# Kernel tuning notes

Hardware: AMD Instinct MI355X
Metric: run time of the kernel (lower is better)

## Reference

```python
import jax, jax.numpy as jnp
import numpy as np

D_MODEL = 768
NUM_HEADS = 12
D_K = D_MODEL // NUM_HEADS
D_FF = 2048
LN_EPS = 1e-3  # Keras LayerNormalization default
B, S = 4, 2048


def layer_norm(x, gamma, beta):
    mu = jnp.mean(x, axis=-1, keepdims=True)
    var = jnp.var(x, axis=-1, keepdims=True)
    return (x - mu) * jax.lax.rsqrt(var + LN_EPS) * gamma + beta


def setup_inputs() -> dict:
    key = jax.random.key(0)
    ks = jax.random.split(key, 16)
    sd = 0.02
    inp = {
        "x": jax.random.normal(ks[0], (B, S, D_MODEL), dtype=jnp.float32),
        "src_mask": jnp.zeros((B, 1, 1, S), dtype=jnp.float32),
        "Wq": jax.random.normal(ks[1], (D_MODEL, D_MODEL), jnp.float32) * sd,
        "bq": jnp.zeros((D_MODEL,), jnp.float32),
        "Wk": jax.random.normal(ks[2], (D_MODEL, D_MODEL), jnp.float32) * sd,
        "bk": jnp.zeros((D_MODEL,), jnp.float32),
        "Wv": jax.random.normal(ks[3], (D_MODEL, D_MODEL), jnp.float32) * sd,
        "bv": jnp.zeros((D_MODEL,), jnp.float32),
        "Wo": jax.random.normal(ks[4], (D_MODEL, D_MODEL), jnp.float32) * sd,
        "bo": jnp.zeros((D_MODEL,), jnp.float32),
        "W1": jax.random.normal(ks[5], (D_MODEL, D_FF), jnp.float32) * sd,
        "b1": jnp.zeros((D_FF,), jnp.float32),
        "W2": jax.random.normal(ks[6], (D_FF, D_MODEL), jnp.float32) * sd,
        "b2": jnp.zeros((D_MODEL,), jnp.float32),
        "gamma1": jnp.ones((D_MODEL,), jnp.float32),
        "beta1": jnp.zeros((D_MODEL,), jnp.float32),
        "gamma2": jnp.ones((D_MODEL,), jnp.float32),
        "beta2": jnp.zeros((D_MODEL,), jnp.float32),
    }
    return inp


def encoder_layer(x, src_mask, Wq, bq, Wk, bk, Wv, bv, Wo, bo, W1, b1, W2, b2,
                  gamma1, beta1, gamma2, beta2):
    b, s, _ = x.shape
    def heads(t):  # [B,S,D] -> [B,H,S,Dk]
        return t.reshape(b, s, NUM_HEADS, D_K).transpose(0, 2, 1, 3)
    Q = heads(x @ Wq + bq)
    K = heads(x @ Wk + bk)
    V = heads(x @ Wv + bv)
    scores = jnp.einsum("bhqd,bhkd->bhqk", Q, K) / jnp.sqrt(jnp.float32(D_K))
    scores = scores + src_mask * (-1e9)
    probs = jax.nn.softmax(scores, axis=-1)
    attn = jnp.einsum("bhqk,bhkd->bhqd", probs, V)
    attn = attn.transpose(0, 2, 1, 3).reshape(b, s, D_MODEL)
    attn_out = attn @ Wo + bo
    # dropout is identity at inference
    x1 = layer_norm(x + attn_out, gamma1, beta1)
    ff = jax.nn.relu(x1 @ W1 + b1) @ W2 + b2
    return layer_norm(x1 + ff, gamma2, beta2)


def reference(x, src_mask, Wq, bq, Wk, bk, Wv, bv, Wo, bo, W1, b1, W2, b2,
              gamma1, beta1, gamma2, beta2):
    return encoder_layer(x, src_mask, Wq, bq, Wk, bk, Wv, bv, Wo, bo,
                         W1, b1, W2, b2, gamma1, beta1, gamma2, beta2)
```

## Files before the change

### kernel.cpp

```cpp
#include <hip/hip_runtime.h>


typedef unsigned short u16;
typedef __bf16 bf16x8 __attribute__((ext_vector_type(8)));
typedef __bf16 bf16x4 __attribute__((ext_vector_type(4)));
typedef unsigned short u16x8 __attribute__((ext_vector_type(8)));
typedef float f32x4 __attribute__((ext_vector_type(4)));

#define D_MODEL 768
#define D_FF    2048
#define NH      12
#define DK      64
#define S_LEN   2048
#define M_TOK   8192

#define QSCALE   0.18033688011112042f
#define MSCALE  -1.4426950408889634e9f

__device__ __forceinline__ float bf2f(u16 v) {
    union { unsigned u; float f; } c; c.u = ((unsigned)v) << 16; return c.f;
}
__device__ __forceinline__ void st_bf(u16* p, float v) { *(__bf16*)p = (__bf16)v; }

__device__ __forceinline__ void gload_lds16(const void* g, void* l) {
    __builtin_amdgcn_global_load_lds(
        (const __attribute__((address_space(1))) void*)g,
        (__attribute__((address_space(3))) void*)l, 16, 0, 0);
}

__global__ __launch_bounds__(256)
void prep_k(const float* __restrict__ x, const float* __restrict__ Wq,
            const float* __restrict__ Wk, const float* __restrict__ Wv,
            const float* __restrict__ Wo, const float* __restrict__ W1,
            const float* __restrict__ W2, u16* __restrict__ xb,
            u16* __restrict__ WqkvT, u16* __restrict__ WoT,
            u16* __restrict__ W1T, u16* __restrict__ W2T) {
    __shared__ float t[32][33];
    const int id = blockIdx.x, tid = threadIdx.x;
    if (id >= 5376) {
        const int i = ((id - 5376) * 256 + tid) * 4;
        const float4 v = *(const float4*)(x + i);
        __bf16 o[4] = {(__bf16)v.x, (__bf16)v.y, (__bf16)v.z, (__bf16)v.w};
        *(bf16x4*)(xb + i) = *(bf16x4*)o;
        return;
    }
    const float* in; u16* out; int R, C, bx, by;
    if (id < 2304) {
        const int z = id / 576, r = id % 576;
        in = z == 0 ? Wq : (z == 1 ? Wk : (z == 2 ? Wv : Wo));
        out = z == 3 ? WoT : WqkvT + z * 768 * 768;
        R = 768; C = 768; bx = (r % 24) * 32; by = (r / 24) * 32;
    } else if (id < 3840) {
        const int r = id - 2304;
        in = W1; out = W1T; R = 768; C = 2048;
        bx = (r % 64) * 32; by = (r / 64) * 32;
    } else {
        const int r = id - 3840;
        in = W2; out = W2T; R = 2048; C = 768;
        bx = (r % 24) * 32; by = (r / 24) * 32;
    }
    const int tx = tid & 31, ty = tid >> 5;
#pragma unroll
    for (int i = 0; i < 32; i += 8)
        t[ty + i][tx] = in[(size_t)(by + ty + i) * C + bx + tx];
    __syncthreads();
#pragma unroll
    for (int i = 0; i < 32; i += 8)
        st_bf(&out[(size_t)(bx + ty + i) * R + by + tx], t[tx][ty + i]);
}

__global__ __launch_bounds__(256, 3)
void qkv_gemm_k(const u16* __restrict__ A, const u16* __restrict__ Bt,
                const float* __restrict__ bq, const float* __restrict__ bk,
                const float* __restrict__ bv, u16* __restrict__ Qb,
                u16* __restrict__ Kb, u16* __restrict__ Vt) {
    __shared__ __align__(16) u16 As[2][128 * 32];
    __shared__ __align__(16) u16 Bs[2][128 * 32];
    const int tid = threadIdx.x;
    const int lane = tid & 63, w = tid >> 6;
    const int r16 = lane & 15, qd = lane >> 4;
    const int qdx = (qd ^ ((r16 >> 1) & 3)) << 3;
    const int m0 = blockIdx.x * 128, n0 = blockIdx.y * 128;
    const int wm = (w & 1) << 6, wn = (w >> 1) << 6;
    const int K = D_MODEL;

    f32x4 acc[4][4] = {};

    const u16* aP[2]; const u16* bP[2]; int f8[2];
#pragma unroll
    for (int it = 0; it < 2; ++it) {
        const int f = it * 256 + tid;
        const int row = f >> 2;
        const int kc = ((f & 3) ^ ((f >> 3) & 3)) << 3;
        aP[it] = A  + (size_t)(m0 + row) * K + kc;
        bP[it] = Bt + (size_t)(n0 + row) * K + kc;
        f8[it] = f * 8;
    }

    for (int k0 = 0; k0 < K; k0 += 64) {
#pragma unroll
        for (int p = 0; p < 2; ++p)
#pragma unroll
            for (int it = 0; it < 2; ++it) {
                gload_lds16(aP[it] + k0 + p * 32, &As[p][f8[it]]);
                gload_lds16(bP[it] + k0 + p * 32, &Bs[p][f8[it]]);
            }
        __syncthreads();
#pragma unroll
        for (int p = 0; p < 2; ++p) {
            bf16x8 af[4], bfr[4];
#pragma unroll
            for (int i = 0; i < 4; ++i) {
                af[i]  = *(const bf16x8*)&As[p][(wm + i * 16 + r16) * 32 + qdx];
                bfr[i] = *(const bf16x8*)&Bs[p][(wn + i * 16 + r16) * 32 + qdx];
            }
#pragma unroll
            for (int i = 0; i < 4; ++i)
#pragma unroll
                for (int j = 0; j < 4; ++j)
                    acc[i][j] = __builtin_amdgcn_mfma_f32_16x16x32_bf16(af[i], bfr[j], acc[i][j], 0, 0, 0);
        }
        __syncthreads();
    }

    const int sel = n0 < 768 ? 0 : (n0 < 1536 ? 1 : 2);
    const float* bias = sel == 0 ? bq : (sel == 1 ? bk : bv);
    const float scale = sel == 0 ? QSCALE : 1.0f;
    const int nbase = n0 - sel * 768;

#pragma unroll
    for (int j = 0; j < 4; ++j) {
        const int ncol = nbase + wn + j * 16 + r16;
        const float bvv = bias[ncol];
#pragma unroll
        for (int i = 0; i < 4; ++i) {
            if (sel == 2) {
                const int h = ncol >> 6, d = ncol & 63;
                const int mb = m0 + wm + i * 16 + qd * 4;
                const int bb = mb >> 11, npb = mb & 2047;
                __bf16 pk[4];
#pragma unroll
                for (int rr = 0; rr < 4; ++rr) pk[rr] = (__bf16)(acc[i][j][rr] + bvv);
                *(bf16x4*)&Vt[(((size_t)(bb * NH + h)) * DK + d) * S_LEN + npb] = *(bf16x4*)pk;
            } else {
#pragma unroll
                for (int rr = 0; rr < 4; ++rr) {
                    const int m = m0 + wm + i * 16 + qd * 4 + rr;
                    const float v = (acc[i][j][rr] + bvv) * scale;
                    if (sel == 0) st_bf(&Qb[(size_t)m * D_MODEL + ncol], v);
                    else          st_bf(&Kb[(size_t)m * D_MODEL + ncol], v);
                }
            }
        }
    }
}

__global__ __launch_bounds__(256, 2)
void g4p_k(const u16* __restrict__ A, const u16* __restrict__ Bt,
           const float* __restrict__ bias, u16* __restrict__ Cout,
           int N, int K) {
    __shared__ __align__(16) u16 AB[2][16384];
    const int tid = threadIdx.x, lane = tid & 63;
    const int w = tid >> 6;
    const int wm2 = w >> 1, wn2 = w & 1;
    const int r16 = lane & 15, qd = lane >> 4;
    const int qdx = (qd ^ ((r16 >> 1) & 3)) << 3;
    const int m0 = blockIdx.x * 128, n0 = blockIdx.y * 128;
    const int NT = K >> 6;

    const u16* aS[4]; const u16* bS[4];
#pragma unroll
    for (int l = 0; l < 4; ++l) {
        const int f = l * 256 + tid;
        const int row = (f >> 2) & 127, ks = f >> 9;
        const int e = (((f & 3) ^ ((f >> 3) & 3)) << 3);
        aS[l] = A  + (size_t)(m0 + row) * K + ks * 32 + e;
        bS[l] = Bt + (size_t)(n0 + row) * K + ks * 32 + e;
    }

#pragma unroll
    for (int l = 0; l < 4; ++l) {
        gload_lds16(aS[l], &AB[0][(l * 256 + tid) * 8]);
        gload_lds16(bS[l], &AB[0][8192 + (l * 256 + tid) * 8]);
    }
    asm volatile("s_waitcnt vmcnt(0)" ::: "memory");
    __builtin_amdgcn_s_barrier();

    f32x4 acc[4][4] = {};
    bf16x8 af[4][2], bfr[4][2];
    const int arow0 = wm2 * 64 + r16;
    const int brow0 = wn2 * 64 + r16;

    for (int t = 0; t < NT; ++t) {
        const int cur = t & 1, nxt = cur ^ 1;
        const u16* ab = AB[cur];
        const int ka = (t + 1) * 64;
        const bool more = (t + 1) < NT;

#pragma unroll
        for (int mt = 0; mt < 4; ++mt)
#pragma unroll
            for (int ks = 0; ks < 2; ++ks)
                af[mt][ks] = *(const bf16x8*)&ab[ks * 4096 + (arow0 + mt * 16) * 32 + qdx];
#pragma unroll
        for (int nt = 0; nt < 2; ++nt)
#pragma unroll
            for (int ks = 0; ks < 2; ++ks)
                bfr[nt][ks] = *(const bf16x8*)&ab[8192 + ks * 4096 + (brow0 + nt * 16) * 32 + qdx];
        if (more) {
#pragma unroll
            for (int l = 0; l < 4; ++l)
                gload_lds16(aS[l] + ka, &AB[nxt][(l * 256 + tid) * 8]);
        }
        __builtin_amdgcn_s_setprio(1);
#pragma unroll
        for (int mt = 0; mt < 4; ++mt)
#pragma unroll
            for (int nt = 0; nt < 2; ++nt)
#pragma unroll
                for (int ks = 0; ks < 2; ++ks)
                    acc[mt][nt] = __builtin_amdgcn_mfma_f32_16x16x32_bf16(bfr[nt][ks], af[mt][ks], acc[mt][nt], 0, 0, 0);
        __builtin_amdgcn_s_setprio(0);
        __builtin_amdgcn_s_barrier();

#pragma unroll
        for (int nt = 2; nt < 4; ++nt)
#pragma unroll
            for (int ks = 0; ks < 2; ++ks)
                bfr[nt][ks] = *(const bf16x8*)&ab[8192 + ks * 4096 + (brow0 + nt * 16) * 32 + qdx];
        if (more) {
#pragma unroll
            for (int l = 0; l < 4; ++l)
                gload_lds16(bS[l] + ka, &AB[nxt][8192 + (l * 256 + tid) * 8]);
        }
        __builtin_amdgcn_s_setprio(1);
#pragma unroll
        for (int mt = 0; mt < 4; ++mt)
#pragma unroll
            for (int nt = 2; nt < 4; ++nt)
#pragma unroll
                for (int ks = 0; ks < 2; ++ks)
                    acc[mt][nt] = __builtin_amdgcn_mfma_f32_16x16x32_bf16(bfr[nt][ks], af[mt][ks], acc[mt][nt], 0, 0, 0);
        __builtin_amdgcn_s_setprio(0);

        if (more) {
            asm volatile("s_waitcnt vmcnt(0)" ::: "memory");
            __builtin_amdgcn_s_barrier();
        }
    }

#pragma unroll
    for (int nt = 0; nt < 4; ++nt) {
        const int nb = n0 + wn2 * 64 + nt * 16 + qd * 4;
        const float4 bv = *(const float4*)&bias[nb];
        const float b4[4] = {bv.x, bv.y, bv.z, bv.w};
#pragma unroll
        for (int mi = 0; mi < 4; ++mi) {
            const int m = m0 + wm2 * 64 + mi * 16 + r16;
            __bf16 pk[4];
#pragma unroll
            for (int rr = 0; rr < 4; ++rr)
                pk[rr] = (__bf16)(acc[mi][nt][rr] + b4[rr]);
            *(bf16x4*)&Cout[(size_t)m * N + nb] = *(bf16x4*)pk;
        }
    }
}

__global__ __launch_bounds__(512, 2)
void ff1_k(const u16* __restrict__ A, const u16* __restrict__ Bt,
           const float* __restrict__ bias, u16* __restrict__ C) {
    __shared__ __align__(16) u16 AB[2][32768];
    const int tid = threadIdx.x, lane = tid & 63;
    const int w = tid >> 6;
    const int wm2 = w >> 2, wn4 = w & 3;
    const int r16 = lane & 15, qd = lane >> 4;
    const int qdx = (qd ^ ((r16 >> 1) & 3)) << 3;
    const int m0 = blockIdx.x * 256, n0 = blockIdx.y * 256;
    const int K = D_MODEL, NT = 12;

    const u16* aS[4]; const u16* bS[4];
#pragma unroll
    for (int l = 0; l < 4; ++l) {
        const int f = l * 512 + tid;
        const int row = (f >> 2) & 255, ks = f >> 10;
        const int e = (((f & 3) ^ ((f >> 3) & 3)) << 3);
        aS[l] = A  + (size_t)(m0 + row) * K + ks * 32 + e;
        bS[l] = Bt + (size_t)(n0 + row) * K + ks * 32 + e;
    }

#pragma unroll
    for (int l = 0; l < 4; ++l) {
        gload_lds16(aS[l], &AB[0][(l * 512 + tid) * 8]);
        gload_lds16(bS[l], &AB[0][16384 + (l * 512 + tid) * 8]);
    }
    asm volatile("s_waitcnt vmcnt(0)" ::: "memory");
    __builtin_amdgcn_s_barrier();

    f32x4 acc[8][4] = {};
    bf16x8 af[4][2], bfr[4][2];
    const int arow0 = wm2 * 128 + r16;
    const int brow0 = wn4 * 64 + r16;

    for (int t = 0; t < NT; ++t) {
        const int cur = t & 1, nxt = cur ^ 1;
        const u16* ab = AB[cur];
        const int ka = (t + 1) * 64;
        const bool more = (t + 1) < NT;

#pragma unroll
        for (int mt = 0; mt < 4; ++mt)
#pragma unroll
            for (int ks = 0; ks < 2; ++ks)
                af[mt][ks] = *(const bf16x8*)&ab[ks * 8192 + (arow0 + mt * 16) * 32 + qdx];
#pragma unroll
        for (int nt = 0; nt < 2; ++nt)
#pragma unroll
            for (int ks = 0; ks < 2; ++ks)
                bfr[nt][ks] = *(const bf16x8*)&ab[16384 + ks * 8192 + (brow0 + nt * 16) * 32 + qdx];
        if (more) {
#pragma unroll
            for (int l = 0; l < 4; ++l)
                gload_lds16(aS[l] + ka, &AB[nxt][(l * 512 + tid) * 8]);
        }
        __builtin_amdgcn_s_setprio(1);
#pragma unroll
        for (int mt = 0; mt < 4; ++mt)
#pragma unroll
            for (int nt = 0; nt < 2; ++nt)
#pragma unroll
                for (int ks = 0; ks < 2; ++ks)
                    acc[mt][nt] = __builtin_amdgcn_mfma_f32_16x16x32_bf16(bfr[nt][ks], af[mt][ks], acc[mt][nt], 0, 0, 0);
        __builtin_amdgcn_s_setprio(0);
        __builtin_amdgcn_s_barrier();

#pragma unroll
        for (int nt = 2; nt < 4; ++nt)
#pragma unroll
            for (int ks = 0; ks < 2; ++ks)
                bfr[nt][ks] = *(const bf16x8*)&ab[16384 + ks * 8192 + (brow0 + nt * 16) * 32 + qdx];
        if (more) {
#pragma unroll
            for (int l = 0; l < 4; ++l)
                gload_lds16(bS[l] + ka, &AB[nxt][16384 + (l * 512 + tid) * 8]);
        }
        __builtin_amdgcn_s_setprio(1);
#pragma unroll
        for (int mt = 0; mt < 4; ++mt)
#pragma unroll
            for (int nt = 2; nt < 4; ++nt)
#pragma unroll
                for (int ks = 0; ks < 2; ++ks)
                    acc[mt][nt] = __builtin_amdgcn_mfma_f32_16x16x32_bf16(bfr[nt][ks], af[mt][ks], acc[mt][nt], 0, 0, 0);
        __builtin_amdgcn_s_setprio(0);
        __builtin_amdgcn_s_barrier();

#pragma unroll
        for (int mt = 0; mt < 4; ++mt)
#pragma unroll
            for (int ks = 0; ks < 2; ++ks)
                af[mt][ks] = *(const bf16x8*)&ab[ks * 8192 + (arow0 + 64 + mt * 16) * 32 + qdx];
        __builtin_amdgcn_s_setprio(1);
#pragma unroll
        for (int mt = 0; mt < 4; ++mt)
#pragma unroll
            for (int nt = 0; nt < 2; ++nt)
#pragma unroll
                for (int ks = 0; ks < 2; ++ks)
                    acc[4 + mt][nt] = __builtin_amdgcn_mfma_f32_16x16x32_bf16(bfr[nt][ks], af[mt][ks], acc[4 + mt][nt], 0, 0, 0);
        __builtin_amdgcn_s_setprio(0);
        __builtin_amdgcn_s_barrier();

        __builtin_amdgcn_s_setprio(1);
#pragma unroll
        for (int mt = 0; mt < 4; ++mt)
#pragma unroll
            for (int nt = 2; nt < 4; ++nt)
#pragma unroll
                for (int ks = 0; ks < 2; ++ks)
                    acc[4 + mt][nt] = __builtin_amdgcn_mfma_f32_16x16x32_bf16(bfr[nt][ks], af[mt][ks], acc[4 + mt][nt], 0, 0, 0);
        __builtin_amdgcn_s_setprio(0);

        if (more) {
            asm volatile("s_waitcnt vmcnt(0)" ::: "memory");
            __builtin_amdgcn_s_barrier();
        }
    }

#pragma unroll
    for (int nt = 0; nt < 4; ++nt) {
        const int nb = n0 + wn4 * 64 + nt * 16 + qd * 4;
        const float4 bv = *(const float4*)&bias[nb];
        const float b4[4] = {bv.x, bv.y, bv.z, bv.w};
#pragma unroll
        for (int mi = 0; mi < 8; ++mi) {
            const int m = m0 + wm2 * 128 + (mi >> 2) * 64 + (mi & 3) * 16 + r16;
            __bf16 pk[4];
#pragma unroll
            for (int rr = 0; rr < 4; ++rr)
                pk[rr] = (__bf16)fmaxf(acc[mi][nt][rr] + b4[rr], 0.0f);
            *(bf16x4*)&C[(size_t)m * D_FF + nb] = *(bf16x4*)pk;
        }
    }
}

#define TS 72

__global__ __launch_bounds__(256, 3)
void attn_k(const u16* __restrict__ Qg, const u16* __restrict__ Kg,
            const u16* __restrict__ Vtg, const float* __restrict__ maskg,
            u16* __restrict__ Og) {
    const int tid = threadIdx.x, lane = tid & 63, w = tid >> 6;
    const int qh = w & 1, kh = w >> 1;
    const int r16 = lane & 15, qd = lane >> 4;
    const int q0 = blockIdx.x * 128;
    const int h = blockIdx.y, b = blockIdx.z;

    __shared__ __align__(16) u16 sm[(64 + 64 + 128) * TS];
    u16* Ks  = sm;
    u16* Vts = sm + 64 * TS;
    u16* Ps  = sm + 128 * TS;

    bf16x8 qa[4][2];
#pragma unroll
    for (int mt = 0; mt < 4; ++mt)
#pragma unroll
        for (int ks = 0; ks < 2; ++ks)
            qa[mt][ks] = *(const bf16x8*)(Qg +
                ((size_t)((b * S_LEN + q0 + qh * 64 + mt * 16 + r16) * NH + h)) * DK +
                ks * 32 + qd * 8);

    const int srow = tid >> 3, sc = (tid & 7) << 3;
    const u16* vsrc = Vtg + (((size_t)(b * NH + h)) * DK) * S_LEN;
    u16x8 kreg[2], vreg[2];
#pragma unroll
    for (int it = 0; it < 2; ++it) {
        const int row = srow + it * 32;
        kreg[it] = *(const u16x8*)(Kg + ((size_t)((b * S_LEN + row) * NH + h)) * DK + sc);
        vreg[it] = *(const u16x8*)(vsrc + (size_t)row * S_LEN + sc);
    }

    float l_i[4] = {0.0f, 0.0f, 0.0f, 0.0f};
    f32x4 Oacc[4][4] = {};

    for (int kt = 0; kt < S_LEN / 64; ++kt) {
        const int ks0 = kt * 64;

#pragma unroll
        for (int it = 0; it < 2; ++it) {
            const int row = srow + it * 32;
            *(u16x8*)&Ks[row * TS + sc]  = kreg[it];
            *(u16x8*)&Vts[row * TS + sc] = vreg[it];
        }

        float4 mrow[2];
#pragma unroll
        for (int nt = 0; nt < 2; ++nt) {
            const float4 mm = ((const float4*)(maskg + (size_t)b * S_LEN + ks0))[kh * 8 + nt * 4 + qd];
            mrow[nt].x = mm.x * MSCALE; mrow[nt].y = mm.y * MSCALE;
            mrow[nt].z = mm.z * MSCALE; mrow[nt].w = mm.w * MSCALE;
        }
        __syncthreads();

        f32x4 sa[4][2];
#pragma unroll
        for (int mt = 0; mt < 4; ++mt)
#pragma unroll
            for (int nt = 0; nt < 2; ++nt) {
                sa[mt][nt][0] = mrow[nt].x; sa[mt][nt][1] = mrow[nt].y;
                sa[mt][nt][2] = mrow[nt].z; sa[mt][nt][3] = mrow[nt].w;
            }
#pragma unroll
        for (int ks = 0; ks < 2; ++ks) {
            bf16x8 kb[2];
#pragma unroll
            for (int nt = 0; nt < 2; ++nt)
                kb[nt] = *(const bf16x8*)&Ks[(kh * 32 + nt * 16 + r16) * TS + ks * 32 + qd * 8];
            __builtin_amdgcn_s_setprio(1);
#pragma unroll
            for (int mt = 0; mt < 4; ++mt)
#pragma unroll
                for (int nt = 0; nt < 2; ++nt)
                    sa[mt][nt] = __builtin_amdgcn_mfma_f32_16x16x32_bf16(kb[nt], qa[mt][ks], sa[mt][nt], 0, 0, 0);
            __builtin_amdgcn_s_setprio(0);
        }

#pragma unroll
        for (int mt = 0; mt < 4; ++mt) {
            float rsum = 0.0f;
#pragma unroll
            for (int nt = 0; nt < 2; ++nt) {
                sa[mt][nt][0] = __builtin_amdgcn_exp2f(sa[mt][nt][0]);
                sa[mt][nt][1] = __builtin_amdgcn_exp2f(sa[mt][nt][1]);
                sa[mt][nt][2] = __builtin_amdgcn_exp2f(sa[mt][nt][2]);
                sa[mt][nt][3] = __builtin_amdgcn_exp2f(sa[mt][nt][3]);
                rsum += sa[mt][nt][0] + sa[mt][nt][1] + sa[mt][nt][2] + sa[mt][nt][3];
            }
            rsum += __shfl_xor(rsum, 16);
            rsum += __shfl_xor(rsum, 32);
            l_i[mt] += rsum;
        }

#pragma unroll
        for (int mt = 0; mt < 4; ++mt)
#pragma unroll
            for (int nt = 0; nt < 2; ++nt) {
                __bf16 pk[4];
#pragma unroll
                for (int rr = 0; rr < 4; ++rr) pk[rr] = (__bf16)sa[mt][nt][rr];
                *(bf16x4*)&Ps[(qh * 64 + mt * 16 + r16) * TS + kh * 32 + nt * 16 + qd * 4] = *(bf16x4*)pk;
            }

        if (kt + 1 < S_LEN / 64) {
            const int ns0 = ks0 + 64;
#pragma unroll
            for (int it = 0; it < 2; ++it) {
                const int row = srow + it * 32;
                kreg[it] = *(const u16x8*)(Kg + ((size_t)((b * S_LEN + ns0 + row) * NH + h)) * DK + sc);
                vreg[it] = *(const u16x8*)(vsrc + (size_t)row * S_LEN + ns0 + sc);
            }
        }

        {
            bf16x8 pa[4], vb[4];
#pragma unroll
            for (int mt = 0; mt < 4; ++mt)
                pa[mt] = *(const bf16x8*)&Ps[(qh * 64 + mt * 16 + r16) * TS + kh * 32 + qd * 8];
#pragma unroll
            for (int vt = 0; vt < 4; ++vt)
                vb[vt] = *(const bf16x8*)&Vts[(vt * 16 + r16) * TS + kh * 32 + qd * 8];
            __builtin_amdgcn_s_setprio(1);
#pragma unroll
            for (int mt = 0; mt < 4; ++mt)
#pragma unroll
                for (int vt = 0; vt < 4; ++vt)
                    Oacc[mt][vt] = __builtin_amdgcn_mfma_f32_16x16x32_bf16(pa[mt], vb[vt], Oacc[mt][vt], 0, 0, 0);
            __builtin_amdgcn_s_setprio(0);
        }
        __syncthreads();
    }

    __syncthreads();
    float* mb  = (float*)sm;
    float* lsm = mb + 128 * 64;
    if (kh == 0) {
#pragma unroll
        for (int mt = 0; mt < 4; ++mt) {
            if (qd == 0) lsm[(qh * 4 + mt) * 16 + r16] = l_i[mt];
#pragma unroll
            for (int vt = 0; vt < 4; ++vt)
#pragma unroll
                for (int rr = 0; rr < 4; ++rr)
                    mb[(qh * 64 + mt * 16 + qd * 4 + rr) * 64 + vt * 16 + r16] = Oacc[mt][vt][rr];
        }
    }
    __syncthreads();
    if (kh == 1) {
#pragma unroll
        for (int mt = 0; mt < 4; ++mt) {
            const float linv = 1.0f / (l_i[mt] + lsm[(qh * 4 + mt) * 16 + r16]);
#pragma unroll
            for (int rr = 0; rr < 4; ++rr) {
                const float lr = __shfl(linv, qd * 4 + rr);
                const int qrow = q0 + qh * 64 + mt * 16 + qd * 4 + rr;
#pragma unroll
                for (int vt = 0; vt < 4; ++vt) {
                    const float o = Oacc[mt][vt][rr] +
                        mb[(qh * 64 + mt * 16 + qd * 4 + rr) * 64 + vt * 16 + r16];
                    st_bf(&Og[((size_t)((b * S_LEN + qrow) * NH + h)) * DK + vt * 16 + r16],
                          o * lr);
                }
            }
        }
    }
}

__global__ __launch_bounds__(256, 4)
void resln_k(const u16* __restrict__ xb, const u16* __restrict__ yb,
             const float* __restrict__ gamma, const float* __restrict__ beta,
             u16* __restrict__ outb, float* __restrict__ outf) {
    const int row = blockIdx.x, tid = threadIdx.x;
    const int lane = tid & 63, w = tid >> 6;
    __shared__ float redS[4], redS2[4];
    const size_t base = (size_t)row * D_MODEL;
    float h[3], s = 0.0f, s2 = 0.0f;
#pragma unroll
    for (int i = 0; i < 3; ++i) {
        const int c = i * 256 + tid;
        const float v = bf2f(xb[base + c]) + bf2f(yb[base + c]);
        h[i] = v; s += v; s2 += v * v;
    }
#pragma unroll
    for (int off = 32; off >= 1; off >>= 1) { s += __shfl_xor(s, off); s2 += __shfl_xor(s2, off); }
    if (lane == 0) { redS[w] = s; redS2[w] = s2; }
    __syncthreads();
    s  = redS[0] + redS[1] + redS[2] + redS[3];
    s2 = redS2[0] + redS2[1] + redS2[2] + redS2[3];
    const float mu  = s * (1.0f / D_MODEL);
    const float var = s2 * (1.0f / D_MODEL) - mu * mu;
    const float rstd = rsqrtf(var + 1e-3f);
#pragma unroll
    for (int i = 0; i < 3; ++i) {
        const int c = i * 256 + tid;
        const float o = (h[i] - mu) * rstd * gamma[c] + beta[c];
        if (outb) st_bf(&outb[base + c], o);
        if (outf) outf[base + c] = o;
    }
}

extern "C" void kernel_launch(void* const* d_in, const int* in_sizes, int n_in,
                              void* d_out, int out_size, void* d_ws, size_t ws_size,
                              hipStream_t stream) {
    (void)in_sizes; (void)n_in; (void)out_size; (void)ws_size;
    const float* x    = (const float*)d_in[0];
    const float* mask = (const float*)d_in[1];
    const float* Wq = (const float*)d_in[2];  const float* bq  = (const float*)d_in[3];
    const float* Wk = (const float*)d_in[4];  const float* bk  = (const float*)d_in[5];
    const float* Wv = (const float*)d_in[6];  const float* bv  = (const float*)d_in[7];
    const float* Wo = (const float*)d_in[8];  const float* bo  = (const float*)d_in[9];
    const float* W1 = (const float*)d_in[10]; const float* b1  = (const float*)d_in[11];
    const float* W2 = (const float*)d_in[12]; const float* b2  = (const float*)d_in[13];
    const float* g1 = (const float*)d_in[14]; const float* be1 = (const float*)d_in[15];
    const float* g2 = (const float*)d_in[16]; const float* be2 = (const float*)d_in[17];

    char* ws = (char*)d_ws;
    u16* xb     = (u16*)(ws + 0);
    u16* WqkvT  = (u16*)(ws + 12582912);
    u16* WoT    = (u16*)(ws + 16121856);
    u16* W1T    = (u16*)(ws + 17301504);
    u16* W2T    = (u16*)(ws + 20447232);
    u16* Qb     = (u16*)(ws + 23592960);
    u16* Kb     = (u16*)(ws + 36175872);
    u16* Vtg    = (u16*)(ws + 48758784);
    u16* Ab     = (u16*)(ws + 61341696);
    u16* Yb     = (u16*)(ws + 73924608);
    u16* X1b    = (u16*)(ws + 86507520);
    u16* H1b    = (u16*)(ws + 23592960);
    u16* Y2b    = (u16*)(ws + 73924608);

    const dim3 blk(256);

    prep_k<<<dim3(11520), blk, 0, stream>>>(x, Wq, Wk, Wv, Wo, W1, W2,
                                            xb, WqkvT, WoT, W1T, W2T);

    qkv_gemm_k<<<dim3(64, 18), blk, 0, stream>>>(xb, WqkvT, bq, bk, bv, Qb, Kb, Vtg);

    attn_k<<<dim3(16, NH, 4), blk, 0, stream>>>(Qb, Kb, Vtg, mask, Ab);

    g4p_k<<<dim3(64, 6), blk, 0, stream>>>(Ab, WoT, bo, Yb, D_MODEL, D_MODEL);

    resln_k<<<dim3(M_TOK), blk, 0, stream>>>(xb, Yb, g1, be1, X1b, nullptr);

    ff1_k<<<dim3(32, 8), dim3(512), 0, stream>>>(X1b, W1T, b1, H1b);

    g4p_k<<<dim3(64, 6), blk, 0, stream>>>(H1b, W2T, b2, Y2b, D_MODEL, D_FF);

    resln_k<<<dim3(M_TOK), blk, 0, stream>>>(X1b, Y2b, g2, be2, nullptr, (float*)d_out);
}
```

Before: 330.5 us.

## Double-buffer QKV GEMM with split-phase prefetch and swapped MFMA operands

Replaces the QKV projection GEMM with a double-buffered, two-phase pipelined version modeled on the existing g4p_k. It prefetches the next K-tile into the alternate LDS buffer while MFMAs run on the current one, and uses s_setprio around the MFMA blocks. MFMA operands are swapped so each lane holds four consecutive output columns, which allows vectorized bias loads and bf16x4 stores for Q and K. The cost is that V transposed stores become scalar, and occupancy drops from 3 to 2 blocks per CU because of the larger LDS buffer.

```diff
diff --git a/kernel.cpp b/kernel.cpp
--- a/kernel.cpp
+++ b/kernel.cpp
@@ -69,58 +69,99 @@
         st_bf(&out[(size_t)(bx + ty + i) * R + by + tx], t[tx][ty + i]);
 }
 
-__global__ __launch_bounds__(256, 3)
-void qkv_gemm_k(const u16* __restrict__ A, const u16* __restrict__ Bt,
-                const float* __restrict__ bq, const float* __restrict__ bk,
-                const float* __restrict__ bv, u16* __restrict__ Qb,
-                u16* __restrict__ Kb, u16* __restrict__ Vt) {
-    __shared__ __align__(16) u16 As[2][128 * 32];
-    __shared__ __align__(16) u16 Bs[2][128 * 32];
-    const int tid = threadIdx.x;
-    const int lane = tid & 63, w = tid >> 6;
+__global__ __launch_bounds__(256, 2)
+void qkv4p_k(const u16* __restrict__ A, const u16* __restrict__ Bt,
+             const float* __restrict__ bq, const float* __restrict__ bk,
+             const float* __restrict__ bv, u16* __restrict__ Qb,
+             u16* __restrict__ Kb, u16* __restrict__ Vt) {
+    __shared__ __align__(16) u16 AB[2][16384];
+    const int tid = threadIdx.x, lane = tid & 63;
+    const int w = tid >> 6;
+    const int wm2 = w >> 1, wn2 = w & 1;
     const int r16 = lane & 15, qd = lane >> 4;
     const int qdx = (qd ^ ((r16 >> 1) & 3)) << 3;
     const int m0 = blockIdx.x * 128, n0 = blockIdx.y * 128;
-    const int wm = (w & 1) << 6, wn = (w >> 1) << 6;
-    const int K = D_MODEL;
+    const int K = D_MODEL, NT = 12;
+
+    const u16* aS[4]; const u16* bS[4];
+#pragma unroll
+    for (int l = 0; l < 4; ++l) {
+        const int f = l * 256 + tid;
+        const int row = (f >> 2) & 127, ks = f >> 9;
+        const int e = (((f & 3) ^ ((f >> 3) & 3)) << 3);
+        aS[l] = A  + (size_t)(m0 + row) * K + ks * 32 + e;
+        bS[l] = Bt + (size_t)(n0 + row) * K + ks * 32 + e;
+    }
+
+#pragma unroll
+    for (int l = 0; l < 4; ++l) {
+        gload_lds16(aS[l], &AB[0][(l * 256 + tid) * 8]);
+        gload_lds16(bS[l], &AB[0][8192 + (l * 256 + tid) * 8]);
+    }
+    asm volatile("s_waitcnt vmcnt(0)" ::: "memory");
+    __builtin_amdgcn_s_barrier();
 
     f32x4 acc[4][4] = {};
-
-    const u16* aP[2]; const u16* bP[2]; int f8[2];
-#pragma unroll
-    for (int it = 0; it < 2; ++it) {
-        const int f = it * 256 + tid;
-        const int row = f >> 2;
-        const int kc = ((f & 3) ^ ((f >> 3) & 3)) << 3;
-        aP[it] = A  + (size_t)(m0 + row) * K + kc;
-        bP[it] = Bt + (size_t)(n0 + row) * K + kc;
-        f8[it] = f * 8;
-    }
-
-    for (int k0 = 0; k0 < K; k0 += 64) {
-#pragma unroll
-        for (int p = 0; p < 2; ++p)
-#pragma unroll
-            for (int it = 0; it < 2; ++it) {
-                gload_lds16(aP[it] + k0 + p * 32, &As[p][f8[it]]);
-                gload_lds16(bP[it] + k0 + p * 32, &Bs[p][f8[it]]);
-            }
-        __syncthreads();
-#pragma unroll
-        for (int p = 0; p < 2; ++p) {
-            bf16x8 af[4], bfr[4];
-#pragma unroll
-            for (int i = 0; i < 4; ++i) {
-                af[i]  = *(const bf16x8*)&As[p][(wm + i * 16 + r16) * 32 + qdx];
-                bfr[i] = *(const bf16x8*)&Bs[p][(wn + i * 16 + r16) * 32 + qdx];
-            }
-#pragma unroll
-            for (int i = 0; i < 4; ++i)
-#pragma unroll
-                for (int j = 0; j < 4; ++j)
-                    acc[i][j] = __builtin_amdgcn_mfma_f32_16x16x32_bf16(af[i], bfr[j], acc[i][j], 0, 0, 0);
-        }
-        __syncthreads();
+    bf16x8 af[4][2], bfr[4][2];
+    const int arow0 = wm2 * 64 + r16;
+    const int brow0 = wn2 * 64 + r16;
+
+    for (int t = 0; t < NT; ++t) {
+        const int cur = t & 1, nxt = cur ^ 1;
+        const u16* ab = AB[cur];
+        const int ka = (t + 1) * 64;
+        const bool more = (t + 1) < NT;
+
+#pragma unroll
+        for (int mt = 0; mt < 4; ++mt)
+#pragma unroll
+            for (int ks = 0; ks < 2; ++ks)
+                af[mt][ks] = *(const bf16x8*)&ab[ks * 4096 + (arow0 + mt * 16) * 32 + qdx];
+#pragma unroll
+        for (int nt = 0; nt < 2; ++nt)
+#pragma unroll
+            for (int ks = 0; ks < 2; ++ks)
+                bfr[nt][ks] = *(const bf16x8*)&ab[8192 + ks * 4096 + (brow0 + nt * 16) * 32 + qdx];
+        if (more) {
+#pragma unroll
+            for (int l = 0; l < 4; ++l)
+                gload_lds16(aS[l] + ka, &AB[nxt][(l * 256 + tid) * 8]);
+        }
+        __builtin_amdgcn_s_setprio(1);
+#pragma unroll
+        for (int mt = 0; mt < 4; ++mt)
+#pragma unroll
+            for (int nt = 0; nt < 2; ++nt)
+#pragma unroll
+                for (int ks = 0; ks < 2; ++ks)
+                    acc[mt][nt] = __builtin_amdgcn_mfma_f32_16x16x32_bf16(bfr[nt][ks], af[mt][ks], acc[mt][nt], 0, 0, 0);
+        __builtin_amdgcn_s_setprio(0);
+        __builtin_amdgcn_s_barrier();
+
+#pragma unroll
+        for (int nt = 2; nt < 4; ++nt)
+#pragma unroll
+            for (int ks = 0; ks < 2; ++ks)
+                bfr[nt][ks] = *(const bf16x8*)&ab[8192 + ks * 4096 + (brow0 + nt * 16) * 32 + qdx];
+        if (more) {
+#pragma unroll
+            for (int l = 0; l < 4; ++l)
+                gload_lds16(bS[l] + ka, &AB[nxt][8192 + (l * 256 + tid) * 8]);
+        }
+        __builtin_amdgcn_s_setprio(1);
+#pragma unroll
+        for (int mt = 0; mt < 4; ++mt)
+#pragma unroll
+            for (int nt = 2; nt < 4; ++nt)
+#pragma unroll
+                for (int ks = 0; ks < 2; ++ks)
+                    acc[mt][nt] = __builtin_amdgcn_mfma_f32_16x16x32_bf16(bfr[nt][ks], af[mt][ks], acc[mt][nt], 0, 0, 0);
+        __builtin_amdgcn_s_setprio(0);
+
+        if (more) {
+            asm volatile("s_waitcnt vmcnt(0)" ::: "memory");
+            __builtin_amdgcn_s_barrier();
+        }
     }
 
     const int sel = n0 < 768 ? 0 : (n0 < 1536 ? 1 : 2);
@@ -129,26 +170,27 @@
     const int nbase = n0 - sel * 768;
 
 #pragma unroll
-    for (int j = 0; j < 4; ++j) {
-        const int ncol = nbase + wn + j * 16 + r16;
-        const float bvv = bias[ncol];
-#pragma unroll
-        for (int i = 0; i < 4; ++i) {
-            if (sel == 2) {
-                const int h = ncol >> 6, d = ncol & 63;
-                const int mb = m0 + wm + i * 16 + qd * 4;
-                const int bb = mb >> 11, npb = mb & 2047;
+    for (int nt = 0; nt < 4; ++nt) {
+        const int nb = nbase + wn2 * 64 + nt * 16 + qd * 4;
+        const float4 bvv = *(const float4*)&bias[nb];
+        const float b4[4] = {bvv.x, bvv.y, bvv.z, bvv.w};
+#pragma unroll
+        for (int mi = 0; mi < 4; ++mi) {
+            const int m = m0 + wm2 * 64 + mi * 16 + r16;
+            if (sel < 2) {
                 __bf16 pk[4];
 #pragma unroll
-                for (int rr = 0; rr < 4; ++rr) pk[rr] = (__bf16)(acc[i][j][rr] + bvv);
-                *(bf16x4*)&Vt[(((size_t)(bb * NH + h)) * DK + d) * S_LEN + npb] = *(bf16x4*)pk;
+                for (int rr = 0; rr < 4; ++rr)
+                    pk[rr] = (__bf16)((acc[mi][nt][rr] + b4[rr]) * scale);
+                u16* dst = (sel == 0 ? Qb : Kb) + (size_t)m * D_MODEL + nb;
+                *(bf16x4*)dst = *(bf16x4*)pk;
             } else {
+                const int bb = m >> 11, npb = m & 2047;
 #pragma unroll
                 for (int rr = 0; rr < 4; ++rr) {
-                    const int m = m0 + wm + i * 16 + qd * 4 + rr;
-                    const float v = (acc[i][j][rr] + bvv) * scale;
-                    if (sel == 0) st_bf(&Qb[(size_t)m * D_MODEL + ncol], v);
-                    else          st_bf(&Kb[(size_t)m * D_MODEL + ncol], v);
+                    const int col = nb + rr, h = col >> 6, d = col & 63;
+                    st_bf(&Vt[(((size_t)(bb * NH + h)) * DK + d) * S_LEN + npb],
+                          acc[mi][nt][rr] + b4[rr]);
                 }
             }
         }
@@ -642,7 +684,7 @@
     prep_k<<<dim3(11520), blk, 0, stream>>>(x, Wq, Wk, Wv, Wo, W1, W2,
                                             xb, WqkvT, WoT, W1T, W2T);
 
-    qkv_gemm_k<<<dim3(64, 18), blk, 0, stream>>>(xb, WqkvT, bq, bk, bv, Qb, Kb, Vtg);
+    qkv4p_k<<<dim3(64, 18), blk, 0, stream>>>(xb, WqkvT, bq, bk, bv, Qb, Kb, Vtg);
 
     attn_k<<<dim3(16, NH, 4), blk, 0, stream>>>(Qb, Kb, Vtg, mask, Ab);
 
```

After: 346.3 us. +4.8%, slower.
